# Kernel tuning notes

Hardware: AMD Instinct MI355X
Metric: run time of the kernel (lower is better)

## Reference

```python
import jax, jax.numpy as jnp
import numpy as np
import math

K = 10  # args.k, hardcoded in order_topk/fast_topk

def sinusoid_pe(seq_len, d_model, dtype=jnp.float32):
    # PositionalEmbedding: pe[:,0::2]=sin(pos*div), pe[:,1::2]=cos(pos*div)
    pos = jnp.arange(seq_len, dtype=jnp.float32)[:, None]
    div = jnp.exp(jnp.arange(0, d_model, 2, dtype=jnp.float32) * (-math.log(10000.0) / d_model))
    ang = pos * div  # [S, d_model//2]
    pe = jnp.zeros((seq_len, d_model), dtype=jnp.float32)
    pe = pe.at[:, 0::2].set(jnp.sin(ang)).at[:, 1::2].set(jnp.cos(ang))
    return pe.astype(dtype)


def setup_inputs() -> dict:
    key = jax.random.key(0)
    ks = jax.random.split(key, 5)
    B, D, S = 128, 512, 512
    scale1 = 1.0 / math.sqrt(2 * D)
    scale2 = 1.0 / math.sqrt(D)
    return {
        "x": jax.random.normal(ks[0], (B, D, S), dtype=jnp.float32),
        "w1": jax.random.normal(ks[1], (2 * D, D), dtype=jnp.float32) * scale1,
        "b1": jax.random.normal(ks[2], (D,), dtype=jnp.float32) * scale1,
        "w2": jax.random.normal(ks[3], (D, 1), dtype=jnp.float32) * scale2,
        "b2": jax.random.normal(ks[4], (1,), dtype=jnp.float32) * scale2,
    }


def reference(x, w1, b1, w2, b2):
    # x: [B, D, S] -> feature: [B, S, D]  (Sampler: x = x.transpose(-1,-2))
    feat = jnp.swapaxes(x, -1, -2)
    B, S, D = feat.shape
    # shot == 1 branch: per-video mean over tokens, broadcast over seq
    info_g = jnp.broadcast_to(feat.mean(axis=-2, keepdims=True), feat.shape)
    h = jnp.concatenate([feat, info_g], axis=-1)  # [B, S, 2D]
    # evaluator: PositionalEmbedding(1024) -> Linear(1024,512) -> ReLU -> Linear(512,1)
    h = h + sinusoid_pe(S, 2 * D, h.dtype)[None]
    score = jax.nn.relu(jnp.einsum('bsf,fd->bsd', h, w1) + b1)
    score = (jnp.einsum('bsd,do->bso', score, w2) + b2)[..., 0]  # [B, S]
    mn = score.min(axis=1, keepdims=True)
    mx = score.max(axis=1, keepdims=True)
    norm_score = (score - mn) / (mx - mn + 1e-4)
    # fast_topk (eval path): top-k indices, sorted ascending, one-hot selection
    _, idx = jax.lax.top_k(norm_score, K)      # [B, K]
    idx = jnp.sort(idx, axis=-1)
    # torch: one_hot -> [B,K,S], .transpose(-1,-2) -> [B,S,K], then indices.transpose(-1,-2) -> [B,K,S]
    indices = jax.nn.one_hot(idx, S, dtype=feat.dtype)  # [B, K, S]
    selected_feature = jnp.einsum('bks,bsd->bkd', indices, feat)  # bmm gather
    return indices, selected_feature, feat
```

## Files before the change

### kernel.cpp

```cpp
#include <hip/hip_runtime.h>
#include <math.h>

#define B 128
#define D 512
#define S 512
#define TOPK 10

typedef short bf16x8 __attribute__((ext_vector_type(8)));
typedef unsigned short u16x8 __attribute__((ext_vector_type(8)));
typedef float f32x4 __attribute__((ext_vector_type(4)));


__device__ __forceinline__ unsigned splitf(float f) {
    unsigned u = __float_as_uint(f);
    unsigned rb = u + 0x7FFFu + ((u >> 16) & 1u);
    float hf = __uint_as_float(rb & 0xFFFF0000u);
    unsigned u2 = __float_as_uint(f - hf);
    return (rb >> 16) | (u2 & 0xFFFF0000u);
}

__device__ __forceinline__ size_t w1t_base(int d, int k) {
    return (size_t)(((d >> 8) * 32 + (k >> 5)) * 4 + ((k >> 3) & 3)) * 4096 +
           (size_t)(d & 255) * 16 + (k & 7);
}

__global__ void zero_kernel(float* __restrict__ p) {
    p[blockIdx.x * 256 + threadIdx.x] = 0.0f;
}

__global__ __launch_bounds__(256) void fused_stage1(
    const float* __restrict__ x, float* __restrict__ feat, float* __restrict__ g,
    ushort* __restrict__ peh, ushort* __restrict__ pel,
    const float* __restrict__ w1, ushort* __restrict__ w1tsw) {
    __shared__ float tile[64 * 65];
    int bid = (int)blockIdx.x;
    int t = threadIdx.x;

    if (bid < 8192) {
        int b = bid >> 6;
        int s0 = (bid & 7) * 64, d0 = ((bid >> 3) & 7) * 64;
        int ty = t >> 4, tx = t & 15;
        const float4* x4 = (const float4*)(x + (size_t)b * D * S);
        float psum[4];
#pragma unroll
        for (int q = 0; q < 4; ++q) {
            int d = ty + 16 * q;
            float4 v = x4[(size_t)(d0 + d) * (S / 4) + (s0 >> 2) + tx];
            tile[d + (4 * tx + 0) * 65] = v.x;
            tile[d + (4 * tx + 1) * 65] = v.y;
            tile[d + (4 * tx + 2) * 65] = v.z;
            tile[d + (4 * tx + 3) * 65] = v.w;
            float sm = (v.x + v.y) + (v.z + v.w);
#pragma unroll
            for (int off = 8; off; off >>= 1) sm += __shfl_down(sm, off, 16);
            psum[q] = sm;
        }
        if (tx == 0) {
#pragma unroll
            for (int q = 0; q < 4; ++q)
                atomicAdd(&g[b * D + d0 + ty + 16 * q], psum[q] * (1.0f / S));
        }
        __syncthreads();
        float4* f4 = (float4*)(feat + (size_t)b * S * D);
#pragma unroll
        for (int q = 0; q < 4; ++q) {
            int s = ty + 16 * q;
            float4 o;
            o.x = tile[(4 * tx + 0) + s * 65];
            o.y = tile[(4 * tx + 1) + s * 65];
            o.z = tile[(4 * tx + 2) + s * 65];
            o.w = tile[(4 * tx + 3) + s * 65];
            f4[(size_t)(s0 + s) * (D / 4) + (d0 >> 2) + tx] = o;
        }
    } else if (bid < 8704) {
        int s = bid - 8192;
#pragma unroll
        for (int q = 0; q < 2; ++q) {
            int i = t + 256 * q;
            float ei = expf((float)(2 * i) * -0.0089944730195f);
            float ang = (float)s * ei;
            float sv = sinf(ang), cv = cosf(ang);
            unsigned ps = splitf(sv), pc = splitf(cv);
            size_t base = (size_t)s * 1024 + 2 * i;
            peh[base] = (ushort)(ps & 0xFFFFu);
            peh[base + 1] = (ushort)(pc & 0xFFFFu);
            pel[base] = (ushort)(ps >> 16);
            pel[base + 1] = (ushort)(pc >> 16);
        }
    } else {
        int id2 = bid - 8704;
        int rp = id2 & 1, tt = id2 >> 1;
        int m = t;
        int d = rp * 256 + m;
        int hs = (m >> 2) & 1;
        ushort* outp = w1tsw + (size_t)(rp * 32 + tt) * 16384 + (size_t)m * 16;
#pragma unroll
        for (int c = 0; c < 4; ++c) {
            u16x8 hi, lo;
#pragma unroll
            for (int j = 0; j < 8; ++j) {
                unsigned p = splitf(w1[(size_t)(tt * 32 + c * 8 + j) * D + d]);
                hi[j] = (ushort)(p & 0xFFFFu);
                lo[j] = (ushort)(p >> 16);
            }
            *(u16x8*)(outp + c * 4096 + hs * 8) = hi;
            *(u16x8*)(outp + c * 4096 + (hs ^ 1) * 8) = lo;
        }
    }
}

#define CP 40
__global__ __launch_bounds__(256) void fused_stage2(
    const float* __restrict__ g, const float* __restrict__ w1, float* __restrict__ gterm,
    const ushort* __restrict__ peh, const ushort* __restrict__ pel,
    const ushort* __restrict__ w1tsw, const float* __restrict__ b1,
    float* __restrict__ C1) {
    __shared__ short smemS[4 * 64 * CP];
    int bid = (int)blockIdx.x;
    int t = threadIdx.x;

    if (bid < 256) {
        int b = bid >> 1, half = bid & 1;
        float* gs = (float*)smemS;
        gs[t] = g[b * D + t];
        gs[t + 256] = g[b * D + 256 + t];
        __syncthreads();
        int d = half * 256 + t;
        float a0 = 0.f, a1 = 0.f, a2 = 0.f, a3 = 0.f;
        for (int k = 0; k < 512; k += 4) {
            a0 += gs[k + 0] * w1[(size_t)(D + k + 0) * D + d];
            a1 += gs[k + 1] * w1[(size_t)(D + k + 1) * D + d];
            a2 += gs[k + 2] * w1[(size_t)(D + k + 2) * D + d];
            a3 += gs[k + 3] * w1[(size_t)(D + k + 3) * D + d];
        }
        gterm[b * D + d] = (a0 + a1) + (a2 + a3);
    } else {
        int cid = bid - 256;
        int d0 = (cid & 7) * 64, s0 = (cid >> 3) * 64;
        short* sAh = smemS;
        short* sAl = smemS + 64 * CP;
        short* sBh = smemS + 2 * 64 * CP;
        short* sBl = smemS + 3 * 64 * CP;
        int w = t >> 6, l = t & 63, lc = l & 15, lg = l >> 4;
        int tm = t >> 2, tk = (t & 3) * 8;
        int bhs = (tm >> 2) & 1;
        f32x4 acc[4] = {};
        for (int k0 = 0; k0 < 1024; k0 += 32) {
            __syncthreads();
            *(bf16x8*)(sAh + tm * CP + tk) =
                *(const bf16x8*)(peh + (size_t)(s0 + tm) * 1024 + k0 + tk);
            *(bf16x8*)(sAl + tm * CP + tk) =
                *(const bf16x8*)(pel + (size_t)(s0 + tm) * 1024 + k0 + tk);
            size_t boff = w1t_base(d0 + tm, k0 + tk);
            *(bf16x8*)(sBh + tm * CP + tk) = *(const bf16x8*)(w1tsw + boff + bhs * 8);
            *(bf16x8*)(sBl + tm * CP + tk) = *(const bf16x8*)(w1tsw + boff + (bhs ^ 1) * 8);
            __syncthreads();
            int m = w * 16 + lc;
            bf16x8 ah = *(const bf16x8*)(sAh + m * CP + lg * 8);
            bf16x8 al = *(const bf16x8*)(sAl + m * CP + lg * 8);
#pragma unroll
            for (int j = 0; j < 4; ++j) {
                int n = j * 16 + lc;
                bf16x8 bh = *(const bf16x8*)(sBh + n * CP + lg * 8);
                bf16x8 bl = *(const bf16x8*)(sBl + n * CP + lg * 8);
                acc[j] = __builtin_amdgcn_mfma_f32_16x16x32_bf16(ah, bh, acc[j], 0, 0, 0);
                acc[j] = __builtin_amdgcn_mfma_f32_16x16x32_bf16(ah, bl, acc[j], 0, 0, 0);
                acc[j] = __builtin_amdgcn_mfma_f32_16x16x32_bf16(al, bh, acc[j], 0, 0, 0);
            }
        }
#pragma unroll
        for (int j = 0; j < 4; ++j)
#pragma unroll
            for (int reg = 0; reg < 4; ++reg) {
                int sg = s0 + w * 16 + lg * 4 + reg;
                int dg = d0 + j * 16 + lc;
                C1[(size_t)sg * D + dg] = acc[j][reg] + b1[dg];
            }
    }
}

__device__ __forceinline__ void gload16(const void* src, void* dst) {
    __builtin_amdgcn_global_load_lds((const __attribute__((address_space(1))) void*)src,
                                     (__attribute__((address_space(3))) void*)dst, 16, 0, 0);
}

__device__ __forceinline__ void split_write(short* sAbuf, int am, int ahalf,
                                            float4 a0, float4 a1, float4 a2, float4 a3) {
    int hs = (am >> 2) & 1;
#pragma unroll
    for (int cc = 0; cc < 2; ++cc) {
        float e0, e1, e2, e3, e4, e5, e6, e7;
        if (cc == 0) {
            e0 = a0.x; e1 = a0.y; e2 = a0.z; e3 = a0.w;
            e4 = a1.x; e5 = a1.y; e6 = a1.z; e7 = a1.w;
        } else {
            e0 = a2.x; e1 = a2.y; e2 = a2.z; e3 = a2.w;
            e4 = a3.x; e5 = a3.y; e6 = a3.z; e7 = a3.w;
        }
        unsigned p0 = splitf(e0), p1 = splitf(e1), p2 = splitf(e2), p3 = splitf(e3);
        unsigned p4 = splitf(e4), p5 = splitf(e5), p6 = splitf(e6), p7 = splitf(e7);
        u16x8 hi, lo;
        hi[0] = (ushort)(p0 & 0xFFFFu); lo[0] = (ushort)(p0 >> 16);
        hi[1] = (ushort)(p1 & 0xFFFFu); lo[1] = (ushort)(p1 >> 16);
        hi[2] = (ushort)(p2 & 0xFFFFu); lo[2] = (ushort)(p2 >> 16);
        hi[3] = (ushort)(p3 & 0xFFFFu); lo[3] = (ushort)(p3 >> 16);
        hi[4] = (ushort)(p4 & 0xFFFFu); lo[4] = (ushort)(p4 >> 16);
        hi[5] = (ushort)(p5 & 0xFFFFu); lo[5] = (ushort)(p5 >> 16);
        hi[6] = (ushort)(p6 & 0xFFFFu); lo[6] = (ushort)(p6 >> 16);
        hi[7] = (ushort)(p7 & 0xFFFFu); lo[7] = (ushort)(p7 >> 16);
        short* dst = sAbuf + (size_t)(2 * ahalf + cc) * 4096 + (size_t)am * 16;
        *(u16x8*)(dst + hs * 8) = hi;
        *(u16x8*)(dst + (hs ^ 1) * 8) = lo;
    }
}

__global__ __launch_bounds__(512, 2) void gemm_mfma(
    const float* __restrict__ feat, const ushort* __restrict__ w1tsw,
    const float* __restrict__ w2, const float* __restrict__ gterm,
    const float* __restrict__ C1, float* __restrict__ score, int row_base) {
    __shared__ short sA[2][4][256][16];
    __shared__ short sB[2][4][256][16];
    int t = threadIdx.x;
    int id = (int)blockIdx.x;
    int lid = (id & 7) * 32 + (id >> 3);
    int rp = lid >> 1, cp = lid & 1;
    int row0 = row_base + (rp << 8);
    int d0 = cp << 8;
    int b = row0 >> 9;

    int am = t & 255, ahalf = t >> 8;
    const float4* asrc = (const float4*)(feat + (size_t)(row0 + am) * D + ahalf * 16);
    const ushort* btile = w1tsw + (size_t)(cp * 32) * 16384;
    int wv = t >> 6, l = t & 63, lc = l & 15, lg = l >> 4;
    int wr = wv >> 1, wc = wv & 1;
    int wbase = (t & ~63);
    int hs = (lc >> 2) & 1;
    int oh = hs * 8, ol = (hs ^ 1) * 8;

    f32x4 acc[4][8] = {};

    {
        float4 a0 = asrc[0], a1 = asrc[1], a2 = asrc[2], a3 = asrc[3];
#pragma unroll
        for (int q = 0; q < 4; ++q)
            gload16(btile + (size_t)(q * 512 + t) * 8,
                    &sB[0][0][0][0] + (size_t)(q * 512 + wbase) * 8);
        split_write(&sA[0][0][0][0], am, ahalf, a0, a1, a2, a3);
    }
    __syncthreads();

    for (int ts = 0; ts < 16; ++ts) {
        int cur = ts & 1, nxt = cur ^ 1;
        float4 a0, a1, a2, a3;
        if (ts < 15) {
            a0 = asrc[(ts + 1) * 8 + 0];
            a1 = asrc[(ts + 1) * 8 + 1];
            a2 = asrc[(ts + 1) * 8 + 2];
            a3 = asrc[(ts + 1) * 8 + 3];
#pragma unroll
            for (int q = 0; q < 4; ++q)
                gload16(btile + (size_t)(ts + 1) * 16384 + (size_t)(q * 512 + t) * 8,
                        &sB[nxt][0][0][0] + (size_t)(q * 512 + wbase) * 8);
        }
        bf16x8 ahf[4], alf[4];
#pragma unroll
        for (int i = 0; i < 4; ++i) {
            const short* ap = &sA[cur][lg][wr * 64 + i * 16 + lc][0];
            ahf[i] = *(const bf16x8*)(ap + oh);
            alf[i] = *(const bf16x8*)(ap + ol);
        }
        __builtin_amdgcn_s_setprio(1);
#pragma unroll
        for (int j = 0; j < 8; ++j) {
            const short* bp = &sB[cur][lg][wc * 128 + j * 16 + lc][0];
            bf16x8 bh = *(const bf16x8*)(bp + oh);
            bf16x8 bl = *(const bf16x8*)(bp + ol);
#pragma unroll
            for (int i = 0; i < 4; ++i) {
                acc[i][j] = __builtin_amdgcn_mfma_f32_16x16x32_bf16(ahf[i], bh, acc[i][j], 0, 0, 0);
                acc[i][j] = __builtin_amdgcn_mfma_f32_16x16x32_bf16(ahf[i], bl, acc[i][j], 0, 0, 0);
                acc[i][j] = __builtin_amdgcn_mfma_f32_16x16x32_bf16(alf[i], bh, acc[i][j], 0, 0, 0);
            }
        }
        __builtin_amdgcn_s_setprio(0);
        if (ts < 15) split_write(&sA[nxt][0][0][0], am, ahalf, a0, a1, a2, a3);
        __syncthreads();
    }

    float w2v[8], gt[8];
#pragma unroll
    for (int j = 0; j < 8; ++j) {
        int d = d0 + wc * 128 + j * 16 + lc;
        w2v[j] = w2[d];
        gt[j] = gterm[b * D + d];
    }
#pragma unroll
    for (int i = 0; i < 4; ++i)
#pragma unroll
        for (int reg = 0; reg < 4; ++reg) {
            int srow = row0 + wr * 64 + i * 16 + lg * 4 + reg;
            int s = srow & 511;
            float part = 0.f;
#pragma unroll
            for (int j = 0; j < 8; ++j) {
                int d = d0 + wc * 128 + j * 16 + lc;
                float z = acc[i][j][reg] + gt[j] + C1[(size_t)s * D + d];
                part += w2v[j] * fmaxf(z, 0.f);
            }
#pragma unroll
            for (int off = 8; off; off >>= 1) part += __shfl_down(part, off, 16);
            if (lc == 0) atomicAdd(&score[srow], part);
        }
}

__global__ void topk_kernel(const float* __restrict__ score, const float* __restrict__ feat,
                            float* __restrict__ out_ind, float* __restrict__ out_sel) {
    __shared__ float work[512];
    __shared__ float wvv[8];
    __shared__ int wii[8];
    __shared__ int topi[TOPK];
    int b = blockIdx.x, t = threadIdx.x;
    work[t] = score[b * S + t];
    __syncthreads();
    for (int it = 0; it < TOPK; ++it) {
        float v = work[t];
        int i = t;
#pragma unroll
        for (int off = 32; off; off >>= 1) {
            float ov = __shfl_down(v, off);
            int oi = __shfl_down(i, off);
            if (ov > v || (ov == v && oi < i)) { v = ov; i = oi; }
        }
        if ((t & 63) == 0) { wvv[t >> 6] = v; wii[t >> 6] = i; }
        __syncthreads();
        if (t == 0) {
            float bv = wvv[0];
            int bi = wii[0];
            for (int w = 1; w < 8; ++w)
                if (wvv[w] > bv || (wvv[w] == bv && wii[w] < bi)) { bv = wvv[w]; bi = wii[w]; }
            topi[it] = bi;
            work[bi] = -INFINITY;
        }
        __syncthreads();
    }
    if (t == 0) {
        for (int a = 1; a < TOPK; ++a) {
            int key = topi[a];
            int c = a - 1;
            while (c >= 0 && topi[c] > key) { topi[c + 1] = topi[c]; --c; }
            topi[c + 1] = key;
        }
    }
    __syncthreads();
    if (t < 128) {
        float4* oi4 = (float4*)(out_ind + (size_t)b * TOPK * S);
        float4* os4 = (float4*)(out_sel + (size_t)b * TOPK * D);
        const float4* fb4 = (const float4*)(feat + (size_t)b * S * D);
#pragma unroll
        for (int k = 0; k < TOPK; ++k) {
            int idx = topi[k];
            float4 ohv;
            ohv.x = (4 * t + 0 == idx) ? 1.0f : 0.0f;
            ohv.y = (4 * t + 1 == idx) ? 1.0f : 0.0f;
            ohv.z = (4 * t + 2 == idx) ? 1.0f : 0.0f;
            ohv.w = (4 * t + 3 == idx) ? 1.0f : 0.0f;
            oi4[k * (S / 4) + t] = ohv;
            os4[k * (D / 4) + t] = fb4[(size_t)idx * (D / 4) + t];
        }
    }
}

extern "C" void kernel_launch(void* const* d_in, const int* in_sizes, int n_in,
                              void* d_out, int out_size, void* d_ws, size_t ws_size,
                              hipStream_t stream) {
    const float* x  = (const float*)d_in[0];
    const float* w1 = (const float*)d_in[1];
    const float* b1 = (const float*)d_in[2];
    const float* w2 = (const float*)d_in[3];

    float* out = (float*)d_out;
    float* out_ind = out;
    float* out_sel = out + (size_t)B * TOPK * S;
    float* feat    = out + 2 * (size_t)B * TOPK * S;

    float* ws      = (float*)d_ws;
    float* g       = ws;
    float* score   = ws + 65536;
    float* gterm   = ws + 131072;
    float* C1      = ws + 196608;
    ushort* w1tsw  = (ushort*)(ws + 458752);
    ushort* peh    = (ushort*)(ws + 983040);
    ushort* pel    = (ushort*)(ws + 1245184);

    zero_kernel<<<512, 256, 0, stream>>>(ws);
    fused_stage1<<<8768, 256, 0, stream>>>(x, feat, g, peh, pel, w1, w1tsw);
    fused_stage2<<<320, 256, 0, stream>>>(g, w1, gterm, peh, pel, w1tsw, b1, C1);
    gemm_mfma<<<256, 512, 0, stream>>>(feat, w1tsw, w2, gterm, C1, score, 0);
    gemm_mfma<<<256, 512, 0, stream>>>(feat, w1tsw, w2, gterm, C1, score, 32768);
    topk_kernel<<<B, 512, 0, stream>>>(score, feat, out_ind, out_sel);
}
```

Before: 418.2 us.

## Replace atomic mean accumulation with partial sums and drop zero kernel

The transpose stage now writes per-s-block partial column means to a workspace buffer instead of using atomicAdd into a zeroed buffer, and stage2 reduces the 8 partials itself. Stage2 also zeroes the score buffer, which removes the separate zero-kernel launch. Stage1 blocks grow to 512 threads with 64x128 tiles and use nontemporal stores for feat, and the PE and W1 prep work is redistributed to match. The cost is extra workspace and extra reads of the partials in stage2.

```diff
diff --git a/kernel.cpp b/kernel.cpp
--- a/kernel.cpp
+++ b/kernel.cpp
@@ -24,78 +24,76 @@
            (size_t)(d & 255) * 16 + (k & 7);
 }
 
-__global__ void zero_kernel(float* __restrict__ p) {
-    p[blockIdx.x * 256 + threadIdx.x] = 0.0f;
-}
-
-__global__ __launch_bounds__(256) void fused_stage1(
-    const float* __restrict__ x, float* __restrict__ feat, float* __restrict__ g,
+__global__ __launch_bounds__(512) void fused_stage1(
+    const float* __restrict__ x, float* __restrict__ feat, float* __restrict__ g_part,
     ushort* __restrict__ peh, ushort* __restrict__ pel,
     const float* __restrict__ w1, ushort* __restrict__ w1tsw) {
-    __shared__ float tile[64 * 65];
+    __shared__ float tile[64 * 129];
     int bid = (int)blockIdx.x;
     int t = threadIdx.x;
 
-    if (bid < 8192) {
-        int b = bid >> 6;
-        int s0 = (bid & 7) * 64, d0 = ((bid >> 3) & 7) * 64;
+    if (bid < 4096) {
+        int b = bid >> 5;
+        int d0 = ((bid >> 3) & 3) * 128;
+        int sblk = bid & 7;
+        int s0 = sblk * 64;
         int ty = t >> 4, tx = t & 15;
         const float4* x4 = (const float4*)(x + (size_t)b * D * S);
         float psum[4];
 #pragma unroll
         for (int q = 0; q < 4; ++q) {
-            int d = ty + 16 * q;
+            int d = ty + 32 * q;
             float4 v = x4[(size_t)(d0 + d) * (S / 4) + (s0 >> 2) + tx];
-            tile[d + (4 * tx + 0) * 65] = v.x;
-            tile[d + (4 * tx + 1) * 65] = v.y;
-            tile[d + (4 * tx + 2) * 65] = v.z;
-            tile[d + (4 * tx + 3) * 65] = v.w;
+            tile[d + (4 * tx + 0) * 129] = v.x;
+            tile[d + (4 * tx + 1) * 129] = v.y;
+            tile[d + (4 * tx + 2) * 129] = v.z;
+            tile[d + (4 * tx + 3) * 129] = v.w;
             float sm = (v.x + v.y) + (v.z + v.w);
 #pragma unroll
             for (int off = 8; off; off >>= 1) sm += __shfl_down(sm, off, 16);
             psum[q] = sm;
         }
         if (tx == 0) {
-#pragma unroll
-            for (int q = 0; q < 4; ++q)
-                atomicAdd(&g[b * D + d0 + ty + 16 * q], psum[q] * (1.0f / S));
+            float* gp = g_part + (size_t)sblk * 65536 + b * D + d0;
+#pragma unroll
+            for (int q = 0; q < 4; ++q) gp[ty + 32 * q] = psum[q] * (1.0f / S);
         }
         __syncthreads();
-        float4* f4 = (float4*)(feat + (size_t)b * S * D);
-#pragma unroll
-        for (int q = 0; q < 4; ++q) {
-            int s = ty + 16 * q;
-            float4 o;
-            o.x = tile[(4 * tx + 0) + s * 65];
-            o.y = tile[(4 * tx + 1) + s * 65];
-            o.z = tile[(4 * tx + 2) + s * 65];
-            o.w = tile[(4 * tx + 3) + s * 65];
-            f4[(size_t)(s0 + s) * (D / 4) + (d0 >> 2) + tx] = o;
-        }
-    } else if (bid < 8704) {
-        int s = bid - 8192;
-#pragma unroll
-        for (int q = 0; q < 2; ++q) {
-            int i = t + 256 * q;
-            float ei = expf((float)(2 * i) * -0.0089944730195f);
-            float ang = (float)s * ei;
-            float sv = sinf(ang), cv = cosf(ang);
-            unsigned ps = splitf(sv), pc = splitf(cv);
-            size_t base = (size_t)s * 1024 + 2 * i;
-            peh[base] = (ushort)(ps & 0xFFFFu);
-            peh[base + 1] = (ushort)(pc & 0xFFFFu);
-            pel[base] = (ushort)(ps >> 16);
-            pel[base + 1] = (ushort)(pc >> 16);
-        }
+        int fx = t & 31, sy = t >> 5;
+        float* fbase = feat + (size_t)b * S * D + d0 + 4 * fx;
+#pragma unroll
+        for (int j = 0; j < 4; ++j) {
+            int s = sy + 16 * j;
+            f32x4 o;
+            o[0] = tile[(4 * fx + 0) + s * 129];
+            o[1] = tile[(4 * fx + 1) + s * 129];
+            o[2] = tile[(4 * fx + 2) + s * 129];
+            o[3] = tile[(4 * fx + 3) + s * 129];
+            __builtin_nontemporal_store(o, (f32x4*)(fbase + (size_t)(s0 + s) * D));
+        }
+    } else if (bid < 4608) {
+        int s = bid - 4096;
+        int i = t;
+        float ei = expf((float)(2 * i) * -0.0089944730195f);
+        float ang = (float)s * ei;
+        float sv = sinf(ang), cv = cosf(ang);
+        unsigned ps = splitf(sv), pc = splitf(cv);
+        size_t base = (size_t)s * 1024 + 2 * i;
+        peh[base] = (ushort)(ps & 0xFFFFu);
+        peh[base + 1] = (ushort)(pc & 0xFFFFu);
+        pel[base] = (ushort)(ps >> 16);
+        pel[base + 1] = (ushort)(pc >> 16);
     } else {
-        int id2 = bid - 8704;
+        int id2 = bid - 4608;
         int rp = id2 & 1, tt = id2 >> 1;
-        int m = t;
+        int m = t & 255;
+        int c0 = (t >> 8) * 2;
         int d = rp * 256 + m;
         int hs = (m >> 2) & 1;
         ushort* outp = w1tsw + (size_t)(rp * 32 + tt) * 16384 + (size_t)m * 16;
 #pragma unroll
-        for (int c = 0; c < 4; ++c) {
+        for (int cc = 0; cc < 2; ++cc) {
+            int c = c0 + cc;
             u16x8 hi, lo;
 #pragma unroll
             for (int j = 0; j < 8; ++j) {
@@ -111,7 +109,8 @@
 
 #define CP 40
 __global__ __launch_bounds__(256) void fused_stage2(
-    const float* __restrict__ g, const float* __restrict__ w1, float* __restrict__ gterm,
+    const float* __restrict__ g_part, const float* __restrict__ w1,
+    float* __restrict__ gterm, float* __restrict__ score,
     const ushort* __restrict__ peh, const ushort* __restrict__ pel,
     const ushort* __restrict__ w1tsw, const float* __restrict__ b1,
     float* __restrict__ C1) {
@@ -120,10 +119,17 @@
     int t = threadIdx.x;
 
     if (bid < 256) {
+        score[bid * 256 + t] = 0.0f;
         int b = bid >> 1, half = bid & 1;
         float* gs = (float*)smemS;
-        gs[t] = g[b * D + t];
-        gs[t + 256] = g[b * D + 256 + t];
+#pragma unroll
+        for (int h = 0; h < 2; ++h) {
+            int k = h * 256 + t;
+            float acc = 0.f;
+#pragma unroll
+            for (int sb = 0; sb < 8; ++sb) acc += g_part[(size_t)sb * 65536 + b * D + k];
+            gs[k] = acc;
+        }
         __syncthreads();
         int d = half * 256 + t;
         float a0 = 0.f, a1 = 0.f, a2 = 0.f, a3 = 0.f;
@@ -384,17 +390,16 @@
     float* feat    = out + 2 * (size_t)B * TOPK * S;
 
     float* ws      = (float*)d_ws;
-    float* g       = ws;
-    float* score   = ws + 65536;
-    float* gterm   = ws + 131072;
-    float* C1      = ws + 196608;
-    ushort* w1tsw  = (ushort*)(ws + 458752);
-    ushort* peh    = (ushort*)(ws + 983040);
-    ushort* pel    = (ushort*)(ws + 1245184);
-
-    zero_kernel<<<512, 256, 0, stream>>>(ws);
-    fused_stage1<<<8768, 256, 0, stream>>>(x, feat, g, peh, pel, w1, w1tsw);
-    fused_stage2<<<320, 256, 0, stream>>>(g, w1, gterm, peh, pel, w1tsw, b1, C1);
+    float* score   = ws;
+    float* gterm   = ws + 65536;
+    float* g_part  = ws + 131072;
+    float* C1      = ws + 655360;
+    ushort* w1tsw  = (ushort*)(ws + 917504);
+    ushort* peh    = (ushort*)(ws + 1441792);
+    ushort* pel    = (ushort*)(ws + 1703936);
+
+    fused_stage1<<<4672, 512, 0, stream>>>(x, feat, g_part, peh, pel, w1, w1tsw);
+    fused_stage2<<<320, 256, 0, stream>>>(g_part, w1, gterm, score, peh, pel, w1tsw, b1, C1);
     gemm_mfma<<<256, 512, 0, stream>>>(feat, w1tsw, w2, gterm, C1, score, 0);
     gemm_mfma<<<256, 512, 0, stream>>>(feat, w1tsw, w2, gterm, C1, score, 32768);
     topk_kernel<<<B, 512, 0, stream>>>(score, feat, out_ind, out_sel);
```

Result: faster. 406.3 us (-2.9%).
